# Kernel optimization log

Measured on AMD Instinct MI355X. Metric: run time of the kernel, lower is better.

Reference implementation:

```python
import jax, jax.numpy as jnp
import numpy as np

D_MODEL = 1024
BATCH = 4
SEQ = 4096


def setup_inputs() -> dict:
    key = jax.random.key(0)
    kx, kq, kk, kv = jax.random.split(key, 4)
    x = jax.random.normal(kx, (BATCH, SEQ, D_MODEL), dtype=jnp.float32)
    s = 1.0 / np.sqrt(D_MODEL)
    w_q = jax.random.normal(kq, (D_MODEL, D_MODEL), dtype=jnp.float32) * s
    w_k = jax.random.normal(kk, (D_MODEL, D_MODEL), dtype=jnp.float32) * s
    w_v = jax.random.normal(kv, (D_MODEL, D_MODEL), dtype=jnp.float32) * s
    # causal mask: 1 = keep, 0 = masked out (matches torch masked_fill(mask==0, -inf))
    mask = jnp.tril(jnp.ones((SEQ, SEQ), dtype=jnp.int32))
    return {"x": x, "w_q": w_q, "w_k": w_k, "w_v": w_v, "mask": mask}


def reference(x, w_q, w_k, w_v, mask):
    # torch nn.Linear: y = x @ W^T
    q = jnp.einsum("bsd,ed->bse", x, w_q)
    k = jnp.einsum("bsd,ed->bse", x, w_k)
    v = jnp.einsum("bsd,ed->bse", x, w_v)
    scale = 1.0 / jnp.sqrt(jnp.asarray(q.shape[-1], dtype=q.dtype))
    scores = jnp.einsum("bqd,bkd->bqk", q, k) * scale  # [B, S, S]
    scores = jnp.where(mask == 0, -jnp.inf, scores)
    attn = jax.nn.softmax(scores, axis=-1)
    return jnp.einsum("bqk,bkd->bqd", attn, v)
```

## Files before the change

### kernel.cpp

```cpp
#include <hip/hip_runtime.h>
#include <stdint.h>


#define DM   1024
#define SEQ  4096
#define NB   4
#define MTOT (NB * SEQ)

typedef unsigned short u16;
typedef unsigned int u32;
typedef __bf16 bf16x8 __attribute__((ext_vector_type(8)));
typedef float f32x4 __attribute__((ext_vector_type(4)));

__device__ __forceinline__ u16 f2bf(float f) {
    u32 u = __float_as_uint(f);
    u32 r = (u + 0x7fffu + ((u >> 16) & 1u)) >> 16;
    return (u16)r;
}

__device__ __forceinline__ void gl_lds16(const void* gptr, void* lptr) {
    __builtin_amdgcn_global_load_lds(
        (const __attribute__((address_space(1))) void*)gptr,
        (__attribute__((address_space(3))) void*)lptr,
        16, 0, 0);
}

__global__ void cvt_kernel(const float* __restrict__ in, u16* __restrict__ out, int n8) {
    int i = blockIdx.x * 256 + threadIdx.x;
    if (i >= n8) return;
    const float4* p = (const float4*)in + (size_t)i * 2;
    float4 a = p[0], b = p[1];
    uint4 o;
    o.x = (u32)f2bf(a.x) | ((u32)f2bf(a.y) << 16);
    o.y = (u32)f2bf(a.z) | ((u32)f2bf(a.w) << 16);
    o.z = (u32)f2bf(b.x) | ((u32)f2bf(b.y) << 16);
    o.w = (u32)f2bf(b.z) | ((u32)f2bf(b.w) << 16);
    ((uint4*)out)[i] = o;
}

__global__ void zero_kernel(float* __restrict__ p, int n) {
    int i = blockIdx.x * 256 + threadIdx.x;
    if (i < n) p[i] = 0.f;
}

__device__ __forceinline__ void gemm_core(
    const u16* __restrict__ A, int lda,
    const u16* __restrict__ B, int ldb,
    int m0, int n0, int kend,
    u16* sA, u16* sB, f32x4 acc[4][4])
{
    const int tid  = threadIdx.x;
    const int lane = tid & 63;
    const int w    = tid >> 6;
    const int wr   = w >> 1, wc = w & 1;
    const int gi   = lane >> 4, fr = lane & 15;
    const int srow = lane >> 2;
    const int scol = (lane & 3) * 8;

    for (int kt = 0; kt < kend; kt += 32) {
#pragma unroll
        for (int r = 0; r < 2; ++r) {
            int c   = w * 2 + r;
            int row = c * 16 + srow;
            gl_lds16(A + (size_t)(m0 + row) * lda + kt + scol, sA + c * 512 + lane * 8);
            gl_lds16(B + (size_t)(n0 + row) * ldb + kt + scol, sB + c * 512 + lane * 8);
        }
        __syncthreads();
        bf16x8 af[4], bq[4];
#pragma unroll
        for (int mi = 0; mi < 4; ++mi)
            af[mi] = *(const bf16x8*)(sA + (wr * 64 + mi * 16 + fr) * 32 + gi * 8);
#pragma unroll
        for (int ni = 0; ni < 4; ++ni)
            bq[ni] = *(const bf16x8*)(sB + (wc * 64 + ni * 16 + fr) * 32 + gi * 8);
#pragma unroll
        for (int mi = 0; mi < 4; ++mi)
#pragma unroll
            for (int ni = 0; ni < 4; ++ni)
                acc[mi][ni] = __builtin_amdgcn_mfma_f32_16x16x32_bf16(
                    af[mi], bq[ni], acc[mi][ni], 0, 0, 0);
        __syncthreads();
    }
}

__global__ __launch_bounds__(256) void qkv_kernel(
    const u16* __restrict__ xb,
    const u16* __restrict__ wq, const u16* __restrict__ wk, const u16* __restrict__ wv,
    u16* __restrict__ Q, u16* __restrict__ K, u16* __restrict__ Vt)
{
    __shared__ __align__(16) u16 sA[128 * 32];
    __shared__ __align__(16) u16 sB[128 * 32];
    const int nt = blockIdx.x;
    const int mt = blockIdx.y;
    const int which = blockIdx.z;
    const u16* W = which == 0 ? wq : which == 1 ? wk : wv;

    f32x4 acc[4][4];
#pragma unroll
    for (int a = 0; a < 4; ++a)
#pragma unroll
        for (int b = 0; b < 4; ++b) acc[a][b] = f32x4{0.f, 0.f, 0.f, 0.f};

    gemm_core(xb, DM, W, DM, mt * 128, nt * 128, DM, sA, sB, acc);

    const int lane = threadIdx.x & 63;
    const int w = threadIdx.x >> 6, wr = w >> 1, wc = w & 1;
    const int gi = lane >> 4, fr = lane & 15;

    if (which < 2) {
        u16* O = which == 0 ? Q : K;
#pragma unroll
        for (int mi = 0; mi < 4; ++mi)
#pragma unroll
            for (int ni = 0; ni < 4; ++ni)
#pragma unroll
                for (int i = 0; i < 4; ++i) {
                    int gm = mt * 128 + wr * 64 + mi * 16 + gi * 4 + i;
                    int gn = nt * 128 + wc * 64 + ni * 16 + fr;
                    O[(size_t)gm * DM + gn] = f2bf(acc[mi][ni][i]);
                }
    } else {
#pragma unroll
        for (int mi = 0; mi < 4; ++mi)
#pragma unroll
            for (int ni = 0; ni < 4; ++ni) {
                int gm = mt * 128 + wr * 64 + mi * 16 + gi * 4;
                int gn = nt * 128 + wc * 64 + ni * 16 + fr;
                int b = gm >> 12, s = gm & (SEQ - 1);
                uint2 pk;
                pk.x = (u32)f2bf(acc[mi][ni][0]) | ((u32)f2bf(acc[mi][ni][1]) << 16);
                pk.y = (u32)f2bf(acc[mi][ni][2]) | ((u32)f2bf(acc[mi][ni][3]) << 16);
                *(uint2*)(Vt + ((size_t)(b * DM + gn)) * SEQ + s) = pk;
            }
    }
}

__global__ __launch_bounds__(256) void scores_kernel(
    const u16* __restrict__ Q, const u16* __restrict__ K,
    u16* __restrict__ P, float* __restrict__ rowsum, int b0)
{
    const int ktile = blockIdx.x, qtile = blockIdx.y, z = blockIdx.z;
    if (ktile > qtile) return;
    const int b = b0 + z;
    const u16* Qb = Q + (size_t)b * SEQ * DM;
    const u16* Kb = K + (size_t)b * SEQ * DM;
    u16* Pb = P + (size_t)z * SEQ * SEQ;

    __shared__ __align__(16) u16 sA[128 * 32];
    __shared__ __align__(16) u16 sB[128 * 32];
    f32x4 acc[4][4];
#pragma unroll
    for (int a = 0; a < 4; ++a)
#pragma unroll
        for (int c = 0; c < 4; ++c) acc[a][c] = f32x4{0.f, 0.f, 0.f, 0.f};

    gemm_core(Qb, DM, Kb, DM, qtile * 128, ktile * 128, DM, sA, sB, acc);

    const int lane = threadIdx.x & 63;
    const int w = threadIdx.x >> 6, wr = w >> 1, wc = w & 1;
    const int gi = lane >> 4, fr = lane & 15;
    const int qt0 = qtile * 128, kt0 = ktile * 128;

#pragma unroll
    for (int mi = 0; mi < 4; ++mi) {
        float rs[4] = {0.f, 0.f, 0.f, 0.f};
#pragma unroll
        for (int ni = 0; ni < 4; ++ni)
#pragma unroll
            for (int i = 0; i < 4; ++i) {
                int gq = qt0 + wr * 64 + mi * 16 + gi * 4 + i;
                int gk = kt0 + wc * 64 + ni * 16 + fr;
                float p = (gk <= gq) ? __expf(acc[mi][ni][i] * 0.03125f) : 0.f;
                Pb[(size_t)gq * SEQ + gk] = f2bf(p);
                rs[i] += p;
            }
#pragma unroll
        for (int i = 0; i < 4; ++i) {
            float s = rs[i];
            s += __shfl_xor(s, 1);
            s += __shfl_xor(s, 2);
            s += __shfl_xor(s, 4);
            s += __shfl_xor(s, 8);
            if (fr == 0) {
                int gq = qt0 + wr * 64 + mi * 16 + gi * 4 + i;
                atomicAdd(&rowsum[(size_t)b * SEQ + gq], s);
            }
        }
    }
}

__global__ __launch_bounds__(256) void pv_kernel(
    const u16* __restrict__ P, const u16* __restrict__ Vt,
    const float* __restrict__ rowsum, float* __restrict__ out, int b0)
{
    const int et = blockIdx.x;
    const int qt = 31 - (int)blockIdx.y;
    const int z = blockIdx.z;
    const int b = b0 + z;
    const u16* Pb = P + (size_t)z * SEQ * SEQ;
    const u16* Vb = Vt + (size_t)b * DM * SEQ;

    __shared__ __align__(16) u16 sA[128 * 32];
    __shared__ __align__(16) u16 sB[128 * 32];
    f32x4 acc[4][4];
#pragma unroll
    for (int a = 0; a < 4; ++a)
#pragma unroll
        for (int c = 0; c < 4; ++c) acc[a][c] = f32x4{0.f, 0.f, 0.f, 0.f};

    const int kend = (qt + 1) * 128;
    gemm_core(Pb, SEQ, Vb, SEQ, qt * 128, et * 128, kend, sA, sB, acc);

    const int lane = threadIdx.x & 63;
    const int w = threadIdx.x >> 6, wr = w >> 1, wc = w & 1;
    const int gi = lane >> 4, fr = lane & 15;

#pragma unroll
    for (int mi = 0; mi < 4; ++mi)
#pragma unroll
        for (int i = 0; i < 4; ++i) {
            int gq = qt * 128 + wr * 64 + mi * 16 + gi * 4 + i;
            float inv = 1.0f / rowsum[(size_t)b * SEQ + gq];
#pragma unroll
            for (int ni = 0; ni < 4; ++ni) {
                int ge = et * 128 + wc * 64 + ni * 16 + fr;
                out[((size_t)b * SEQ + gq) * DM + ge] = acc[mi][ni][i] * inv;
            }
        }
}

extern "C" void kernel_launch(void* const* d_in, const int* in_sizes, int n_in,
                              void* d_out, int out_size, void* d_ws, size_t ws_size,
                              hipStream_t stream)
{
    const float* x  = (const float*)d_in[0];
    const float* wq = (const float*)d_in[1];
    const float* wk = (const float*)d_in[2];
    const float* wv = (const float*)d_in[3];
    float* out = (float*)d_out;
    char* ws = (char*)d_ws;
    const size_t MB = 1u << 20;

    auto need = [&](int g) {
        return (size_t)(32 * g + 96 + 6) * MB + (size_t)(NB * SEQ * 4) + 65536;
    };
    int g = (ws_size >= need(4)) ? 4 : (ws_size >= need(2)) ? 2 : 1;

    size_t off = 0;
    u16* P  = (u16*)(ws);            off += (size_t)32 * MB * g;
    u16* xb = (u16*)(ws);
    u16* Q  = (u16*)(ws + off);      off += 32 * MB;
    u16* K  = (u16*)(ws + off);      off += 32 * MB;
    u16* Vt = (u16*)(ws + off);      off += 32 * MB;
    u16* wqb = (u16*)(ws + off);     off += 2 * MB;
    u16* wkb = (u16*)(ws + off);     off += 2 * MB;
    u16* wvb = (u16*)(ws + off);     off += 2 * MB;
    float* rowsum = (float*)(ws + off);

    cvt_kernel<<<(MTOT * DM / 8) / 256, 256, 0, stream>>>(x, xb, MTOT * DM / 8);
    cvt_kernel<<<(DM * DM / 8) / 256, 256, 0, stream>>>(wq, wqb, DM * DM / 8);
    cvt_kernel<<<(DM * DM / 8) / 256, 256, 0, stream>>>(wk, wkb, DM * DM / 8);
    cvt_kernel<<<(DM * DM / 8) / 256, 256, 0, stream>>>(wv, wvb, DM * DM / 8);
    zero_kernel<<<(NB * SEQ) / 256, 256, 0, stream>>>(rowsum, NB * SEQ);

    qkv_kernel<<<dim3(8, 128, 3), 256, 0, stream>>>(xb, wqb, wkb, wvb, Q, K, Vt);

    for (int b0 = 0; b0 < NB; b0 += g) {
        scores_kernel<<<dim3(32, 32, g), 256, 0, stream>>>(Q, K, P, rowsum, b0);
        pv_kernel<<<dim3(8, 32, g), 256, 0, stream>>>(P, Vt, rowsum, out, b0);
    }
}
```

Baseline: 604.3 us.

## Replace GEMM core with 256x256 tiled, double-buffered, LDS-swizzled pipelined kernel

Replaces the simple 128x128, K=32 synchronous GEMM loop with a 256x256 tile, K=64 version run by 512 threads. It double-buffers LDS, issues global-to-LDS loads interleaved with MFMA phases, XOR-swizzles the LDS layout to avoid bank conflicts, and raises wave priority around the MFMA blocks. The goal is to hide global memory latency and raise arithmetic intensity for the QKV, scores and PV GEMMs. In exchange it uses 128KB of LDS and one block per CU, and the coarser tiles waste more work along the causal diagonal.

```diff
diff --git a/kernel.cpp b/kernel.cpp
--- a/kernel.cpp
+++ b/kernel.cpp
@@ -43,89 +43,186 @@
     if (i < n) p[i] = 0.f;
 }
 
-__device__ __forceinline__ void gemm_core(
-    const u16* __restrict__ A, int lda,
-    const u16* __restrict__ B, int ldb,
-    int m0, int n0, int kend,
-    u16* sA, u16* sB, f32x4 acc[4][4])
-{
+
+#define S0A_OFF 0
+#define S0B_OFF 16384
+#define S1A_OFF 32768
+#define S1B_OFF 49152
+
+__device__ __forceinline__ void stage_half(const u16* __restrict__ G, int ldg,
+                                           int row0, int kt, u16* ldsop, int h,
+                                           int tid) {
+    int r    = h * 128 + (tid >> 3);
+    int ecol = (tid & 7) * 8;
+    int esrc = ecol ^ (((tid >> 3) & 7) << 3);
+    gl_lds16(G + (size_t)(row0 + r) * ldg + kt + esrc,      ldsop + r * 64 + ecol);
+    gl_lds16(G + (size_t)(row0 + r + 64) * ldg + kt + esrc, ldsop + (r + 64) * 64 + ecol);
+}
+
+__device__ __forceinline__ bf16x8 lds_ld(const u16* base, int byteoff) {
+    return *(const bf16x8*)((const char*)base + byteoff);
+}
+
+__device__ __forceinline__ void gemm256(const u16* __restrict__ A, int lda,
+                                        const u16* __restrict__ B, int ldb,
+                                        int m0, int n0, int NT,
+                                        u16* lds, f32x4 acc[8][4]) {
     const int tid  = threadIdx.x;
     const int lane = tid & 63;
     const int w    = tid >> 6;
-    const int wr   = w >> 1, wc = w & 1;
+    const int wr   = w >> 2, wc = w & 3;
     const int gi   = lane >> 4, fr = lane & 15;
-    const int srow = lane >> 2;
-    const int scol = (lane & 3) * 8;
-
-    for (int kt = 0; kt < kend; kt += 32) {
-#pragma unroll
-        for (int r = 0; r < 2; ++r) {
-            int c   = w * 2 + r;
-            int row = c * 16 + srow;
-            gl_lds16(A + (size_t)(m0 + row) * lda + kt + scol, sA + c * 512 + lane * 8);
-            gl_lds16(B + (size_t)(n0 + row) * ldb + kt + scol, sB + c * 512 + lane * 8);
+    const int key  = (fr & 7) << 4;
+    const int cx0  = (gi * 16) ^ key;
+    const int cx1  = (gi * 16 + 64) ^ key;
+    const int rAb  = (wr * 128 + fr) * 128;
+    const int rBb  = (wc * 64 + fr) * 128;
+
+    u16* s0A = lds + S0A_OFF;
+    u16* s0B = lds + S0B_OFF;
+    u16* s1A = lds + S1A_OFF;
+    u16* s1B = lds + S1B_OFF;
+
+    stage_half(B, ldb, n0, 0,  s0B, 0, tid);
+    stage_half(B, ldb, n0, 0,  s0B, 1, tid);
+    stage_half(A, lda, m0, 0,  s0A, 0, tid);
+    stage_half(A, lda, m0, 0,  s0A, 1, tid);
+    stage_half(B, ldb, n0, 64, s1B, 0, tid);
+    stage_half(B, ldb, n0, 64, s1B, 1, tid);
+    asm volatile("s_waitcnt vmcnt(4)" ::: "memory");
+    __builtin_amdgcn_sched_barrier(0);
+    __builtin_amdgcn_s_barrier();
+
+    bf16x8 b[4][2];
+    bf16x8 af[2][2];
+
+    const int nt2 = NT >> 1;
+    for (int i = 0; i < nt2; ++i) {
+        const int t    = 2 * i;
+        const int more = (t + 2 < NT);
+#pragma unroll
+        for (int p = 0; p < 4; ++p) {
+            if (p == 0) {
+#pragma unroll
+                for (int ni = 0; ni < 4; ++ni) {
+                    b[ni][0] = lds_ld(s0B, rBb + ni * 2048 + cx0);
+                    b[ni][1] = lds_ld(s0B, rBb + ni * 2048 + cx1);
+                }
+            }
+            af[0][0] = lds_ld(s0A, rAb + (2 * p + 0) * 2048 + cx0);
+            af[0][1] = lds_ld(s0A, rAb + (2 * p + 0) * 2048 + cx1);
+            af[1][0] = lds_ld(s0A, rAb + (2 * p + 1) * 2048 + cx0);
+            af[1][1] = lds_ld(s0A, rAb + (2 * p + 1) * 2048 + cx1);
+            if (p == 0) stage_half(A, lda, m0, (t + 1) * 64, s1A, 0, tid);
+            if (p == 1) { stage_half(A, lda, m0, (t + 1) * 64, s1A, 1, tid);
+                          if (more) stage_half(B, ldb, n0, (t + 2) * 64, s0B, 0, tid); }
+            if (p == 2) { if (more) stage_half(B, ldb, n0, (t + 2) * 64, s0B, 1, tid); }
+            __builtin_amdgcn_s_barrier();
+            asm volatile("s_waitcnt lgkmcnt(0)" ::: "memory");
+            __builtin_amdgcn_sched_barrier(0);
+            __builtin_amdgcn_s_setprio(1);
+#pragma unroll
+            for (int j = 0; j < 2; ++j)
+#pragma unroll
+                for (int ni = 0; ni < 4; ++ni) {
+                    acc[2 * p + j][ni] = __builtin_amdgcn_mfma_f32_16x16x32_bf16(
+                        af[j][0], b[ni][0], acc[2 * p + j][ni], 0, 0, 0);
+                    acc[2 * p + j][ni] = __builtin_amdgcn_mfma_f32_16x16x32_bf16(
+                        af[j][1], b[ni][1], acc[2 * p + j][ni], 0, 0, 0);
+                }
+            __builtin_amdgcn_s_setprio(0);
+            if (p == 3) {
+                if (more) { asm volatile("s_waitcnt vmcnt(4)" ::: "memory"); }
+                else      { asm volatile("s_waitcnt vmcnt(0)" ::: "memory"); }
+                __builtin_amdgcn_sched_barrier(0);
+            }
+            __builtin_amdgcn_s_barrier();
+            __builtin_amdgcn_sched_barrier(0);
         }
-        __syncthreads();
-        bf16x8 af[4], bq[4];
-#pragma unroll
-        for (int mi = 0; mi < 4; ++mi)
-            af[mi] = *(const bf16x8*)(sA + (wr * 64 + mi * 16 + fr) * 32 + gi * 8);
-#pragma unroll
-        for (int ni = 0; ni < 4; ++ni)
-            bq[ni] = *(const bf16x8*)(sB + (wc * 64 + ni * 16 + fr) * 32 + gi * 8);
-#pragma unroll
-        for (int mi = 0; mi < 4; ++mi)
-#pragma unroll
-            for (int ni = 0; ni < 4; ++ni)
-                acc[mi][ni] = __builtin_amdgcn_mfma_f32_16x16x32_bf16(
-                    af[mi], bq[ni], acc[mi][ni], 0, 0, 0);
-        __syncthreads();
+#pragma unroll
+        for (int p = 0; p < 4; ++p) {
+            if (p == 0) {
+#pragma unroll
+                for (int ni = 0; ni < 4; ++ni) {
+                    b[ni][0] = lds_ld(s1B, rBb + ni * 2048 + cx0);
+                    b[ni][1] = lds_ld(s1B, rBb + ni * 2048 + cx1);
+                }
+            }
+            af[0][0] = lds_ld(s1A, rAb + (2 * p + 0) * 2048 + cx0);
+            af[0][1] = lds_ld(s1A, rAb + (2 * p + 0) * 2048 + cx1);
+            af[1][0] = lds_ld(s1A, rAb + (2 * p + 1) * 2048 + cx0);
+            af[1][1] = lds_ld(s1A, rAb + (2 * p + 1) * 2048 + cx1);
+            if (p == 0) { if (more) stage_half(A, lda, m0, (t + 2) * 64, s0A, 0, tid); }
+            if (p == 1) { if (more) { stage_half(A, lda, m0, (t + 2) * 64, s0A, 1, tid);
+                                      stage_half(B, ldb, n0, (t + 3) * 64, s1B, 0, tid); } }
+            if (p == 2) { if (more) stage_half(B, ldb, n0, (t + 3) * 64, s1B, 1, tid); }
+            __builtin_amdgcn_s_barrier();
+            asm volatile("s_waitcnt lgkmcnt(0)" ::: "memory");
+            __builtin_amdgcn_sched_barrier(0);
+            __builtin_amdgcn_s_setprio(1);
+#pragma unroll
+            for (int j = 0; j < 2; ++j)
+#pragma unroll
+                for (int ni = 0; ni < 4; ++ni) {
+                    acc[2 * p + j][ni] = __builtin_amdgcn_mfma_f32_16x16x32_bf16(
+                        af[j][0], b[ni][0], acc[2 * p + j][ni], 0, 0, 0);
+                    acc[2 * p + j][ni] = __builtin_amdgcn_mfma_f32_16x16x32_bf16(
+                        af[j][1], b[ni][1], acc[2 * p + j][ni], 0, 0, 0);
+                }
+            __builtin_amdgcn_s_setprio(0);
+            if (p == 3 && more) {
+                asm volatile("s_waitcnt vmcnt(4)" ::: "memory");
+                __builtin_amdgcn_sched_barrier(0);
+            }
+            __builtin_amdgcn_s_barrier();
+            __builtin_amdgcn_sched_barrier(0);
+        }
     }
 }
 
-__global__ __launch_bounds__(256) void qkv_kernel(
+#define ACC_INIT(acc)                                                        \
+    _Pragma("unroll") for (int a_ = 0; a_ < 8; ++a_)                         \
+    _Pragma("unroll") for (int b_ = 0; b_ < 4; ++b_)                         \
+        acc[a_][b_] = f32x4{0.f, 0.f, 0.f, 0.f};
+
+__global__ __launch_bounds__(512, 1) void qkv_kernel(
     const u16* __restrict__ xb,
     const u16* __restrict__ wq, const u16* __restrict__ wk, const u16* __restrict__ wv,
     u16* __restrict__ Q, u16* __restrict__ K, u16* __restrict__ Vt)
 {
-    __shared__ __align__(16) u16 sA[128 * 32];
-    __shared__ __align__(16) u16 sB[128 * 32];
+    __shared__ __align__(16) u16 lds[65536];
     const int nt = blockIdx.x;
     const int mt = blockIdx.y;
     const int which = blockIdx.z;
     const u16* W = which == 0 ? wq : which == 1 ? wk : wv;
 
-    f32x4 acc[4][4];
-#pragma unroll
-    for (int a = 0; a < 4; ++a)
-#pragma unroll
-        for (int b = 0; b < 4; ++b) acc[a][b] = f32x4{0.f, 0.f, 0.f, 0.f};
-
-    gemm_core(xb, DM, W, DM, mt * 128, nt * 128, DM, sA, sB, acc);
+    f32x4 acc[8][4];
+    ACC_INIT(acc);
+    gemm256(xb, DM, W, DM, mt * 256, nt * 256, DM / 64, lds, acc);
 
     const int lane = threadIdx.x & 63;
-    const int w = threadIdx.x >> 6, wr = w >> 1, wc = w & 1;
+    const int w = threadIdx.x >> 6, wr = w >> 2, wc = w & 3;
     const int gi = lane >> 4, fr = lane & 15;
 
     if (which < 2) {
         u16* O = which == 0 ? Q : K;
 #pragma unroll
-        for (int mi = 0; mi < 4; ++mi)
+        for (int mi = 0; mi < 8; ++mi)
 #pragma unroll
             for (int ni = 0; ni < 4; ++ni)
 #pragma unroll
                 for (int i = 0; i < 4; ++i) {
-                    int gm = mt * 128 + wr * 64 + mi * 16 + gi * 4 + i;
-                    int gn = nt * 128 + wc * 64 + ni * 16 + fr;
+                    int gm = mt * 256 + wr * 128 + mi * 16 + gi * 4 + i;
+                    int gn = nt * 256 + wc * 64 + ni * 16 + fr;
                     O[(size_t)gm * DM + gn] = f2bf(acc[mi][ni][i]);
                 }
     } else {
 #pragma unroll
-        for (int mi = 0; mi < 4; ++mi)
+        for (int mi = 0; mi < 8; ++mi)
 #pragma unroll
             for (int ni = 0; ni < 4; ++ni) {
-                int gm = mt * 128 + wr * 64 + mi * 16 + gi * 4;
-                int gn = nt * 128 + wc * 64 + ni * 16 + fr;
+                int gm = mt * 256 + wr * 128 + mi * 16 + gi * 4;
+                int gn = nt * 256 + wc * 64 + ni * 16 + fr;
                 int b = gm >> 12, s = gm & (SEQ - 1);
                 uint2 pk;
                 pk.x = (u32)f2bf(acc[mi][ni][0]) | ((u32)f2bf(acc[mi][ni][1]) << 16);
@@ -135,7 +232,7 @@
     }
 }
 
-__global__ __launch_bounds__(256) void scores_kernel(
+__global__ __launch_bounds__(512, 1) void scores_kernel(
     const u16* __restrict__ Q, const u16* __restrict__ K,
     u16* __restrict__ P, float* __restrict__ rowsum, int b0)
 {
@@ -146,29 +243,24 @@
     const u16* Kb = K + (size_t)b * SEQ * DM;
     u16* Pb = P + (size_t)z * SEQ * SEQ;
 
-    __shared__ __align__(16) u16 sA[128 * 32];
-    __shared__ __align__(16) u16 sB[128 * 32];
-    f32x4 acc[4][4];
-#pragma unroll
-    for (int a = 0; a < 4; ++a)
-#pragma unroll
-        for (int c = 0; c < 4; ++c) acc[a][c] = f32x4{0.f, 0.f, 0.f, 0.f};
-
-    gemm_core(Qb, DM, Kb, DM, qtile * 128, ktile * 128, DM, sA, sB, acc);
+    __shared__ __align__(16) u16 lds[65536];
+    f32x4 acc[8][4];
+    ACC_INIT(acc);
+    gemm256(Qb, DM, Kb, DM, qtile * 256, ktile * 256, DM / 64, lds, acc);
 
     const int lane = threadIdx.x & 63;
-    const int w = threadIdx.x >> 6, wr = w >> 1, wc = w & 1;
+    const int w = threadIdx.x >> 6, wr = w >> 2, wc = w & 3;
     const int gi = lane >> 4, fr = lane & 15;
-    const int qt0 = qtile * 128, kt0 = ktile * 128;
-
-#pragma unroll
-    for (int mi = 0; mi < 4; ++mi) {
+    const int qt0 = qtile * 256, kt0 = ktile * 256;
+
+#pragma unroll
+    for (int mi = 0; mi < 8; ++mi) {
         float rs[4] = {0.f, 0.f, 0.f, 0.f};
 #pragma unroll
         for (int ni = 0; ni < 4; ++ni)
 #pragma unroll
             for (int i = 0; i < 4; ++i) {
-                int gq = qt0 + wr * 64 + mi * 16 + gi * 4 + i;
+                int gq = qt0 + wr * 128 + mi * 16 + gi * 4 + i;
                 int gk = kt0 + wc * 64 + ni * 16 + fr;
                 float p = (gk <= gq) ? __expf(acc[mi][ni][i] * 0.03125f) : 0.f;
                 Pb[(size_t)gq * SEQ + gk] = f2bf(p);
@@ -182,48 +274,43 @@
             s += __shfl_xor(s, 4);
             s += __shfl_xor(s, 8);
             if (fr == 0) {
-                int gq = qt0 + wr * 64 + mi * 16 + gi * 4 + i;
+                int gq = qt0 + wr * 128 + mi * 16 + gi * 4 + i;
                 atomicAdd(&rowsum[(size_t)b * SEQ + gq], s);
             }
         }
     }
 }
 
-__global__ __launch_bounds__(256) void pv_kernel(
+__global__ __launch_bounds__(512, 1) void pv_kernel(
     const u16* __restrict__ P, const u16* __restrict__ Vt,
     const float* __restrict__ rowsum, float* __restrict__ out, int b0)
 {
     const int et = blockIdx.x;
-    const int qt = 31 - (int)blockIdx.y;
+    const int qt = 15 - (int)blockIdx.y;
     const int z = blockIdx.z;
     const int b = b0 + z;
     const u16* Pb = P + (size_t)z * SEQ * SEQ;
     const u16* Vb = Vt + (size_t)b * DM * SEQ;
 
-    __shared__ __align__(16) u16 sA[128 * 32];
-    __shared__ __align__(16) u16 sB[128 * 32];
-    f32x4 acc[4][4];
-#pragma unroll
-    for (int a = 0; a < 4; ++a)
-#pragma unroll
-        for (int c = 0; c < 4; ++c) acc[a][c] = f32x4{0.f, 0.f, 0.f, 0.f};
-
-    const int kend = (qt + 1) * 128;
-    gemm_core(Pb, SEQ, Vb, SEQ, qt * 128, et * 128, kend, sA, sB, acc);
+    __shared__ __align__(16) u16 lds[65536];
+    f32x4 acc[8][4];
+    ACC_INIT(acc);
+    const int NT = (qt + 1) * 4;
+    gemm256(Pb, SEQ, Vb, SEQ, qt * 256, et * 256, NT, lds, acc);
 
     const int lane = threadIdx.x & 63;
-    const int w = threadIdx.x >> 6, wr = w >> 1, wc = w & 1;
+    const int w = threadIdx.x >> 6, wr = w >> 2, wc = w & 3;
     const int gi = lane >> 4, fr = lane & 15;
 
 #pragma unroll
-    for (int mi = 0; mi < 4; ++mi)
+    for (int mi = 0; mi < 8; ++mi)
 #pragma unroll
         for (int i = 0; i < 4; ++i) {
-            int gq = qt * 128 + wr * 64 + mi * 16 + gi * 4 + i;
+            int gq = qt * 256 + wr * 128 + mi * 16 + gi * 4 + i;
             float inv = 1.0f / rowsum[(size_t)b * SEQ + gq];
 #pragma unroll
             for (int ni = 0; ni < 4; ++ni) {
-                int ge = et * 128 + wc * 64 + ni * 16 + fr;
+                int ge = et * 256 + wc * 64 + ni * 16 + fr;
                 out[((size_t)b * SEQ + gq) * DM + ge] = acc[mi][ni][i] * inv;
             }
         }
@@ -263,10 +350,10 @@
     cvt_kernel<<<(DM * DM / 8) / 256, 256, 0, stream>>>(wv, wvb, DM * DM / 8);
     zero_kernel<<<(NB * SEQ) / 256, 256, 0, stream>>>(rowsum, NB * SEQ);
 
-    qkv_kernel<<<dim3(8, 128, 3), 256, 0, stream>>>(xb, wqb, wkb, wvb, Q, K, Vt);
+    qkv_kernel<<<dim3(4, 64, 3), 512, 0, stream>>>(xb, wqb, wkb, wvb, Q, K, Vt);
 
     for (int b0 = 0; b0 < NB; b0 += g) {
-        scores_kernel<<<dim3(32, 32, g), 256, 0, stream>>>(Q, K, P, rowsum, b0);
-        pv_kernel<<<dim3(8, 32, g), 256, 0, stream>>>(P, Vt, rowsum, out, b0);
+        scores_kernel<<<dim3(16, 16, g), 512, 0, stream>>>(Q, K, P, rowsum, b0);
+        pv_kernel<<<dim3(4, 16, g), 512, 0, stream>>>(P, Vt, rowsum, out, b0);
     }
 }
```

Measured after the change: 525.0 us. 13.1% less time.
